# Kernel tuning notes

Measured on AMD Instinct MI355X. Metric: run time of the kernel, lower is better.

## Reference

```python
import jax, jax.numpy as jnp
import numpy as np

EPS = 1e-5
NUM_HEADS = 4


def _layer_norm(x, g, b):
    m = jnp.mean(x, axis=-1, keepdims=True)
    v = jnp.mean((x - m) ** 2, axis=-1, keepdims=True)
    return (x - m) / jnp.sqrt(v + EPS) * g + b


def setup_inputs() -> dict:
    key = jax.random.key(0)
    ks = jax.random.split(key, 32)
    B, N, ND, TD, L = 100000, 20, 128, 64, 2
    HD = 128  # num_heads * attention_dim
    CD = ND + TD  # 192
    s = 0.02
    inp = {
        "node_features": jax.random.normal(ks[0], (B, ND), jnp.float32),
        "neighbor_features": jax.random.normal(ks[1], (B, N, ND), jnp.float32),
        "node_times": jax.random.uniform(ks[2], (B,), jnp.float32),
        "neighbor_times": jax.random.uniform(ks[3], (B, N), jnp.float32),
        "time_freq": jax.random.normal(ks[4], (TD,), jnp.float32),
        "time_phase": jnp.zeros((TD,), jnp.float32),
        "Wq": jax.random.normal(ks[5], (L, CD, HD), jnp.float32) * s,
        "bq": jnp.zeros((L, HD), jnp.float32),
        "Wk": jax.random.normal(ks[6], (L, CD, HD), jnp.float32) * s,
        "bk": jnp.zeros((L, HD), jnp.float32),
        "Wv": jax.random.normal(ks[7], (L, CD, HD), jnp.float32) * s,
        "bv": jnp.zeros((L, HD), jnp.float32),
        "Wo": jax.random.normal(ks[8], (L, HD, ND), jnp.float32) * s,
        "bo": jnp.zeros((L, ND), jnp.float32),
        "W1": jax.random.normal(ks[9], (L, ND, 2 * ND), jnp.float32) * s,
        "b1": jnp.zeros((L, 2 * ND), jnp.float32),
        "W2": jax.random.normal(ks[10], (L, 2 * ND, ND), jnp.float32) * s,
        "b2": jnp.zeros((L, ND), jnp.float32),
        "g1": jnp.ones((L, ND), jnp.float32),
        "be1": jnp.zeros((L, ND), jnp.float32),
        "g2": jnp.ones((L, ND), jnp.float32),
        "be2": jnp.zeros((L, ND), jnp.float32),
        "Wc1": jax.random.normal(ks[11], (ND, ND // 2), jnp.float32) * s,
        "bc1": jnp.zeros((ND // 2,), jnp.float32),
        "Wc2": jax.random.normal(ks[12], (ND // 2, 1), jnp.float32) * s,
        "bc2": jnp.zeros((1,), jnp.float32),
        "mask": jax.random.randint(ks[13], (B, N), 0, 2, jnp.int32),
    }
    return inp


def reference(node_features, neighbor_features, node_times, neighbor_times,
              time_freq, time_phase, Wq, bq, Wk, bk, Wv, bv, Wo, bo,
              W1, b1, W2, b2, g1, be1, g2, be2, Wc1, bc1, Wc2, bc2, mask):
    L, _, HD = Wq.shape
    B, N, ND = neighbor_features.shape
    H = NUM_HEADS
    D = HD // H
    scale = 1.0 / np.sqrt(D).astype(np.float32)
    # time encodings (Bochner): cos(t * w + phi)
    tq = jnp.cos(node_times[:, None] * time_freq + time_phase)          # [B, TD]
    tk = jnp.cos(neighbor_times[..., None] * time_freq + time_phase)   # [B, N, TD]
    kcomb = jnp.concatenate([neighbor_features, tk], axis=-1)           # [B, N, CD]
    pad = (mask == 0)[:, None, :]                                       # [B, 1, N]
    x = node_features
    for l in range(L):
        qcomb = jnp.concatenate([x, tq], axis=-1)                       # [B, CD]
        q = (qcomb @ Wq[l] + bq[l]).reshape(B, H, D)
        k = (kcomb @ Wk[l] + bk[l]).reshape(B, N, H, D)
        v = (kcomb @ Wv[l] + bv[l]).reshape(B, N, H, D)
        scores = jnp.einsum('bhd,bnhd->bhn', q, k) * scale              # [B, H, N]
        scores = jnp.where(pad, jnp.float32(-1e9), scores)
        w = jax.nn.softmax(scores, axis=-1)
        a = jnp.einsum('bhn,bnhd->bhd', w, v).reshape(B, HD)
        attn = a @ Wo[l] + bo[l]                                        # [B, ND]
        x = _layer_norm(x + attn, g1[l], be1[l])
        ff = jax.nn.relu(x @ W1[l] + b1[l]) @ W2[l] + b2[l]
        x = _layer_norm(x + ff, g2[l], be2[l])
    h = jax.nn.relu(x @ Wc1 + bc1)
    return jax.nn.sigmoid(h @ Wc2 + bc2)                                # [B, 1]
```

## Files before the change

kernel.cpp:

```cpp
#include <hip/hip_runtime.h>

#define BB 100000
#define NN 20
#define ND 128
#define TD 64
#define CD 192
#define HD 128
#define NH 4
#define DH 32
#define NL 2

typedef __attribute__((ext_vector_type(8))) short bf16x8;
typedef __attribute__((ext_vector_type(4))) float f32x4;

static __device__ __forceinline__ float bf2f(unsigned short u) {
  return __uint_as_float(((unsigned)u) << 16);
}
static __device__ __forceinline__ unsigned short f2bf(float x) {
  unsigned b = __float_as_uint(x);
  return (unsigned short)((b + 0x7FFFu + ((b >> 16) & 1u)) >> 16);
}
static __device__ __forceinline__ bf16x8 load_a8(const float* p) {
  float4 a = *(const float4*)p, b = *(const float4*)(p + 4);
  bf16x8 r;
  r[0] = (short)f2bf(a.x); r[1] = (short)f2bf(a.y);
  r[2] = (short)f2bf(a.z); r[3] = (short)f2bf(a.w);
  r[4] = (short)f2bf(b.x); r[5] = (short)f2bf(b.y);
  r[6] = (short)f2bf(b.z); r[7] = (short)f2bf(b.w);
  return r;
}


__global__ __launch_bounds__(256) void conv_w(
    const float* __restrict__ Wq, const float* __restrict__ Wk,
    const float* __restrict__ Wv, const float* __restrict__ Wo,
    const float* __restrict__ W1, const float* __restrict__ W2,
    unsigned short* __restrict__ WF) {
  int t = blockIdx.x;
  int l = t / 304, tt = t % 304;
#pragma unroll
  for (int e = 0; e < 2; ++e) {
    int idx = threadIdx.x * 2 + e;
    int lane = idx >> 3, j = idx & 7;
    int wk = ((lane >> 4) << 3) + j;
    int c16 = lane & 15;
    float v;
    if (tt < 48) {
      int kt = tt >> 3, n2 = tt & 7;
      v = Wq[((size_t)l * CD + kt * 32 + wk) * HD + n2 * 16 + c16];
    } else if (tt < 96) {
      int t2 = tt - 48; int h = t2 / 12, n2 = t2 % 12;
      v = Wk[((size_t)l * CD + n2 * 16 + c16) * HD + h * 32 + wk];
    } else if (tt < 144) {
      int t2 = tt - 96; int h = t2 / 12, r2 = t2 % 12, kt = r2 >> 1, n2 = r2 & 1;
      v = Wv[((size_t)l * CD + kt * 32 + wk) * HD + h * 32 + n2 * 16 + c16];
    } else if (tt < 176) {
      int t2 = tt - 144; int kt = t2 >> 3, n2 = t2 & 7;
      v = Wo[((size_t)l * HD + kt * 32 + wk) * ND + n2 * 16 + c16];
    } else if (tt < 240) {
      int t2 = tt - 176; int kt = t2 >> 4, n2 = t2 & 15;
      v = W1[((size_t)l * ND + kt * 32 + wk) * (2 * ND) + n2 * 16 + c16];
    } else {
      int t2 = tt - 240; int kt = t2 >> 3, n2 = t2 & 7;
      v = W2[((size_t)l * 2 * ND + kt * 32 + wk) * ND + n2 * 16 + c16];
    }
    WF[(size_t)l * 155648 + (size_t)tt * 512 + idx] = f2bf(v);
  }
}

__global__ __launch_bounds__(256) void prep_tq(
    const float* __restrict__ ntime, const float* __restrict__ tf,
    const float* __restrict__ tp, float* __restrict__ tqf) {
  int i = blockIdx.x * 256 + threadIdx.x;
  int b = i >> 6, j = i & 63;
  tqf[i] = __cosf(ntime[b] * tf[j] + tp[j]);
}

__global__ __launch_bounds__(256) void prep_mb(const int* __restrict__ mask,
                                               unsigned* __restrict__ mb) {
  int e = blockIdx.x * 256 + threadIdx.x;
  if (e < BB) {
    unsigned m = 0;
    for (int n = 0; n < NN; ++n)
      m |= (mask[(size_t)e * NN + n] != 0 ? 1u : 0u) << n;
    mb[e] = m;
  }
}

template <int TN, int ABF, int OBF>
__global__ __launch_bounds__(256) void gemm16(
    const void* __restrict__ A, int lda,
    const float* __restrict__ A2, int lda2, int ksplit,
    const unsigned short* __restrict__ BF,
    int ktiles, int ntiles, int aKoffMul, int cColMul, int segBMul,
    const float* __restrict__ bias,
    void* __restrict__ C, int ldc, int relu) {
  const int tid = threadIdx.x;
  const int wv = tid >> 6, lane = tid & 63;
  const int NW = blockDim.x >> 6;
  const int m0 = blockIdx.x << 4;
  const int seg = blockIdx.y;
  const int arow = m0 + (lane & 15);
  const int kgrp = (lane >> 4) << 3;
  const int aK = seg * aKoffMul;
  const unsigned short* Bseg = BF + (size_t)seg * segBMul * 512;
  f32x4 acc[TN];
#pragma unroll
  for (int i = 0; i < TN; ++i) acc[i] = f32x4{0.f, 0.f, 0.f, 0.f};
  for (int kt = 0; kt < ktiles; ++kt) {
    bf16x8 af;
    if (kt * 32 >= ksplit) {
      af = load_a8(A2 + (size_t)arow * lda2 + (kt * 32 - ksplit) + kgrp);
    } else if (ABF) {
      af = *(const bf16x8*)((const unsigned short*)A + (size_t)arow * lda + aK +
                            kt * 32 + kgrp);
    } else {
      af = load_a8((const float*)A + (size_t)arow * lda + aK + kt * 32 + kgrp);
    }
#pragma unroll
    for (int i = 0; i < TN; ++i) {
      int nt = wv + NW * i;
      bf16x8 bf = *(const bf16x8*)(Bseg + (((size_t)(kt * ntiles + nt)) << 9) +
                                   (lane << 3));
      acc[i] = __builtin_amdgcn_mfma_f32_16x16x32_bf16(af, bf, acc[i], 0, 0, 0);
    }
  }
  const int crow = m0 + ((lane >> 4) << 2);
#pragma unroll
  for (int i = 0; i < TN; ++i) {
    int nt = wv + NW * i;
    int col = seg * cColMul + nt * 16 + (lane & 15);
    float bv = bias ? bias[col] : 0.f;
#pragma unroll
    for (int rr = 0; rr < 4; ++rr) {
      float v = acc[i][rr] + bv;
      if (relu) v = fmaxf(v, 0.f);
      if (OBF)
        ((unsigned short*)C)[(size_t)(crow + rr) * ldc + col] = f2bf(v);
      else
        ((float*)C)[(size_t)(crow + rr) * ldc + col] = v;
    }
  }
}

template <int ABF>
__global__ __launch_bounds__(256) void gemm_ln(
    const void* __restrict__ A, int lda, int ktiles,
    const unsigned short* __restrict__ BF,
    const float* __restrict__ bias, const float* __restrict__ res,
    const float* __restrict__ gamma, const float* __restrict__ beta,
    float* __restrict__ xout) {
  __shared__ float Cs[16][132];
  const int tid = threadIdx.x;
  const int wv = tid >> 6, lane = tid & 63;
  const int m0 = blockIdx.x << 4;
  const int arow = m0 + (lane & 15);
  const int kgrp = (lane >> 4) << 3;
  const int nt0 = wv, nt1 = wv + 4;
  f32x4 acc0 = {0.f, 0.f, 0.f, 0.f}, acc1 = {0.f, 0.f, 0.f, 0.f};
  for (int kt = 0; kt < ktiles; ++kt) {
    bf16x8 af;
    if (ABF)
      af = *(const bf16x8*)((const unsigned short*)A + (size_t)arow * lda +
                            kt * 32 + kgrp);
    else
      af = load_a8((const float*)A + (size_t)arow * lda + kt * 32 + kgrp);
    bf16x8 b0 = *(const bf16x8*)(BF + (((size_t)(kt * 8 + nt0)) << 9) + (lane << 3));
    bf16x8 b1 = *(const bf16x8*)(BF + (((size_t)(kt * 8 + nt1)) << 9) + (lane << 3));
    acc0 = __builtin_amdgcn_mfma_f32_16x16x32_bf16(af, b0, acc0, 0, 0, 0);
    acc1 = __builtin_amdgcn_mfma_f32_16x16x32_bf16(af, b1, acc1, 0, 0, 0);
  }
  {
    const int lrow = (lane >> 4) << 2;
    int c0 = nt0 * 16 + (lane & 15), c1 = nt1 * 16 + (lane & 15);
    float bv0 = bias[c0], bv1 = bias[c1];
#pragma unroll
    for (int rr = 0; rr < 4; ++rr) {
      Cs[lrow + rr][c0] = acc0[rr] + bv0;
      Cs[lrow + rr][c1] = acc1[rr] + bv1;
    }
  }
  __syncthreads();
#pragma unroll
  for (int rr = 0; rr < 4; ++rr) {
    int rw = wv * 4 + rr;
    size_t grow = (size_t)(m0 + rw) * ND;
    float y0 = Cs[rw][lane] + res[grow + lane];
    float y1 = Cs[rw][lane + 64] + res[grow + lane + 64];
    float s = y0 + y1, ss = y0 * y0 + y1 * y1;
#pragma unroll
    for (int off = 32; off > 0; off >>= 1) {
      s += __shfl_xor(s, off);
      ss += __shfl_xor(ss, off);
    }
    float mean = s * (1.f / ND);
    float var = ss * (1.f / ND) - mean * mean;
    float rstd = rsqrtf(var + 1e-5f);
    xout[grow + lane] = (y0 - mean) * rstd * gamma[lane] + beta[lane];
    xout[grow + lane + 64] =
        (y1 - mean) * rstd * gamma[lane + 64] + beta[lane + 64];
  }
}

template <int KCSRC>
__global__ __launch_bounds__(256) void attn_t(
    const float* __restrict__ nbf, const float* __restrict__ nbt,
    const float* __restrict__ tf, const float* __restrict__ tp,
    const unsigned short* __restrict__ kcf_in,
    unsigned short* __restrict__ kcf_out,
    const unsigned* __restrict__ mb, const unsigned short* __restrict__ r,
    unsigned short* __restrict__ u) {
  __shared__ __align__(16) unsigned short kcb[2][NN][200];
  __shared__ __align__(16) float rs[2][768];
  __shared__ __align__(16) float scs[2][NH][NN];
  __shared__ unsigned msks[2];
  const int tid = threadIdx.x;
  const size_t e0 = (size_t)blockIdx.x * 2;

  if (tid < 192) {
    uint4 v = *(const uint4*)(r + e0 * 768 + tid * 8);
    const unsigned short* pv = (const unsigned short*)&v;
    float* dst = &rs[0][0] + tid * 8;
#pragma unroll
    for (int k = 0; k < 8; ++k) dst[k] = bf2f(pv[k]);
  }
  if (KCSRC == 2) {
    for (int i = tid; i < 960; i += 256) {
      int el = i / 480, rem = i % 480;
      int n = rem / 24, q = rem % 24;
      *(uint4*)&kcb[el][n][q * 8] =
          *(const uint4*)&kcf_in[((e0 + el) * NN + n) * 192 + q * 8];
    }
  } else {
    for (int i = tid; i < 2 * NN * 32; i += 256) {
      int el = i / (NN * 32), rem = i % (NN * 32);
      int n = rem >> 5, cq = rem & 31;
      float4 v = *(const float4*)&nbf[((e0 + el) * NN + n) * ND + cq * 4];
      ushort4 o;
      o.x = f2bf(v.x); o.y = f2bf(v.y); o.z = f2bf(v.z); o.w = f2bf(v.w);
      *(ushort4*)&kcb[el][n][cq * 4] = o;
      if (KCSRC == 1)
        *(ushort4*)&kcf_out[((e0 + el) * NN + n) * 192 + cq * 4] = o;
    }
    for (int i = tid; i < 2 * NN * 32; i += 256) {
      int el = i / (NN * 32), rem = i % (NN * 32);
      int n = rem >> 5, jp = (rem & 31) * 2;
      float t = nbt[(e0 + el) * NN + n];
      unsigned a = f2bf(__cosf(t * tf[jp] + tp[jp]));
      unsigned b = f2bf(__cosf(t * tf[jp + 1] + tp[jp + 1]));
      unsigned w = a | (b << 16);
      *(unsigned*)&kcb[el][n][ND + jp] = w;
      if (KCSRC == 1)
        *(unsigned*)&kcf_out[((e0 + el) * NN + n) * 192 + ND + jp] = w;
    }
  }
  if (tid < 2) msks[tid] = mb[e0 + tid];
  __syncthreads();
  if (tid < 2 * NH * NN) {
    int el = tid / (NH * NN), rem = tid % (NH * NN);
    int h = rem / NN, n = rem % NN;
    const float* rp = &rs[el][h * CD];
    const unsigned short* kp = &kcb[el][n][0];
    float acc = 0.f;
    for (int c = 0; c < CD; c += 4) {
      float4 rv = *(const float4*)&rp[c];
      ushort4 kv = *(const ushort4*)&kp[c];
      acc += rv.x * bf2f(kv.x) + rv.y * bf2f(kv.y) + rv.z * bf2f(kv.z) +
             rv.w * bf2f(kv.w);
    }
    scs[el][h][n] =
        ((msks[el] >> n) & 1u) ? acc * 0.17677669529663687f : -1e9f;
  }
  __syncthreads();
  if (tid < 2 * NH) {
    int el = tid >> 2, h = tid & 3;
    float mx = -3.4e38f;
#pragma unroll
    for (int n = 0; n < NN; ++n) mx = fmaxf(mx, scs[el][h][n]);
    float ev[NN], s = 0.f;
#pragma unroll
    for (int n = 0; n < NN; ++n) { ev[n] = __expf(scs[el][h][n] - mx); s += ev[n]; }
    float inv = 1.f / s;
#pragma unroll
    for (int n = 0; n < NN; ++n) scs[el][h][n] = ev[n] * inv;
  }
  __syncthreads();
  for (int i = tid; i < 2 * NH * (CD / 4); i += 256) {
    int el = i / (NH * 48), rem = i % (NH * 48);
    int h = rem / 48, cq = (rem % 48) * 4;
    float a0 = 0.f, a1 = 0.f, a2 = 0.f, a3 = 0.f;
#pragma unroll
    for (int n = 0; n < NN; ++n) {
      float w = scs[el][h][n];
      ushort4 kv = *(const ushort4*)&kcb[el][n][cq];
      a0 += w * bf2f(kv.x); a1 += w * bf2f(kv.y);
      a2 += w * bf2f(kv.z); a3 += w * bf2f(kv.w);
    }
    ushort4 o;
    o.x = f2bf(a0); o.y = f2bf(a1); o.z = f2bf(a2); o.w = f2bf(a3);
    *(ushort4*)&u[(e0 + el) * 768 + h * 192 + cq] = o;
  }
}

__global__ __launch_bounds__(256) void cls_k(
    const float* __restrict__ xf, const float* __restrict__ Wc1,
    const float* __restrict__ bc1, const float* __restrict__ Wc2,
    const float* __restrict__ bc2, float* __restrict__ out) {
  __shared__ float xsh[4][128];
  const int tid = threadIdx.x;
  const size_t e0 = (size_t)blockIdx.x * 4;
  for (int i = tid; i < 512; i += 256) xsh[0][i] = xf[e0 * 128 + i];
  __syncthreads();
  int el = tid >> 6, lane = tid & 63;
  float acc = 0.f;
  for (int c = 0; c < 128; ++c) acc += xsh[el][c] * Wc1[c * 64 + lane];
  acc = fmaxf(acc + bc1[lane], 0.f);
  float p = acc * Wc2[lane];
#pragma unroll
  for (int off = 32; off > 0; off >>= 1) p += __shfl_xor(p, off);
  if (lane == 0) out[e0 + el] = 1.f / (1.f + expf(-(p + bc2[0])));
}

#define G 2
#define T 256
#define KCS 196
#define RUS 772

__global__ __launch_bounds__(T, 4) void tgat_fused(
    const float* __restrict__ nf, const float* __restrict__ nbf,
    const float* __restrict__ nt, const float* __restrict__ nbt,
    const float* __restrict__ tf, const float* __restrict__ tp,
    const float* __restrict__ Wq, const float* __restrict__ bq,
    const float* __restrict__ Wk,
    const float* __restrict__ Wv, const float* __restrict__ bv,
    const float* __restrict__ Wo, const float* __restrict__ bo,
    const float* __restrict__ W1, const float* __restrict__ b1,
    const float* __restrict__ W2, const float* __restrict__ b2,
    const float* __restrict__ g1, const float* __restrict__ be1,
    const float* __restrict__ g2, const float* __restrict__ be2,
    const float* __restrict__ Wc1, const float* __restrict__ bc1,
    const float* __restrict__ Wc2, const float* __restrict__ bc2,
    const int* __restrict__ mask,
    float* __restrict__ out) {
  __shared__ __align__(16) unsigned short kc[G][NN][KCS];
  __shared__ __align__(16) float xs[G][ND];
  __shared__ __align__(16) float tqs[G][TD];
  __shared__ __align__(16) float ys[G][HD];
  __shared__ __align__(16) float rus[G][RUS];
  __shared__ __align__(16) float scs[G][NH][NN];
  __shared__ __align__(16) float h1s[G][2 * ND];
  __shared__ __align__(16) unsigned msks[G];
  float* asv = &h1s[0][0];
  const int tid = threadIdx.x;
  const int b0 = blockIdx.x * G;
  {
    int g = tid >> 7, j = tid & 127;
    xs[g][j] = nf[(b0 + g) * ND + j];
  }
  if (tid < G * TD) {
    int g = tid >> 6, j = tid & 63;
    tqs[g][j] = __cosf(nt[b0 + g] * tf[j] + tp[j]);
  }
  if (tid < G) {
    unsigned m = 0;
    for (int n = 0; n < NN; ++n)
      m |= (mask[(b0 + tid) * NN + n] != 0 ? 1u : 0u) << n;
    msks[tid] = m;
  }
  for (int idx = tid; idx < G * NN * (ND / 4); idx += T) {
    int g = idx / (NN * 32), rem = idx % (NN * 32);
    int n = rem >> 5, cq = rem & 31;
    float4 v = *(const float4*)&nbf[(((b0 + g) * NN + n) * ND) + cq * 4];
    ushort4 o;
    o.x = f2bf(v.x); o.y = f2bf(v.y); o.z = f2bf(v.z); o.w = f2bf(v.w);
    *(ushort4*)&kc[g][n][cq * 4] = o;
  }
  for (int idx = tid; idx < G * NN * TD; idx += T) {
    int g = idx / (NN * TD), rem = idx % (NN * TD);
    int n = rem >> 6, j = rem & 63;
    kc[g][n][ND + j] = f2bf(__cosf(nbt[(b0 + g) * NN + n] * tf[j] + tp[j]));
  }
  __syncthreads();
  const float scale = 0.17677669529663687f;
  for (int l = 0; l < NL; ++l) {
    {
      int g = tid >> 7, j = tid & 127;
      const float* wq = Wq + (l * CD) * HD + j;
      float acc = bq[l * HD + j];
      for (int c = 0; c < CD; c += 4) {
        float4 qv = (c < ND) ? *(const float4*)&xs[g][c]
                             : *(const float4*)&tqs[g][c - ND];
        acc += qv.x * wq[(c + 0) * HD] + qv.y * wq[(c + 1) * HD] +
               qv.z * wq[(c + 2) * HD] + qv.w * wq[(c + 3) * HD];
      }
      ys[g][j] = acc;
    }
    __syncthreads();
    for (int rep = 0; rep < 3; ++rep) {
      int i = rep * T + tid;
      int h = i / CD;
      int c2 = i - h * CD;
      const float* wk = Wk + (l * CD + c2) * HD + h * DH;
      const float* yp0 = &ys[0][h * DH];
      const float* yp1 = &ys[1][h * DH];
      float a0 = 0.f, a1 = 0.f;
#pragma unroll
      for (int d = 0; d < DH; d += 4) {
        float4 w4 = *(const float4*)&wk[d];
        float4 y0 = *(const float4*)&yp0[d];
        float4 y1 = *(const float4*)&yp1[d];
        a0 += y0.x * w4.x + y0.y * w4.y + y0.z * w4.z + y0.w * w4.w;
        a1 += y1.x * w4.x + y1.y * w4.y + y1.z * w4.z + y1.w * w4.w;
      }
      rus[0][i] = a0;
      rus[1][i] = a1;
    }
    __syncthreads();
    if (tid < G * NH * NN) {
      int g = tid / (NH * NN), rem = tid % (NH * NN);
      int h = rem / NN, n = rem % NN;
      const float* rp = &rus[g][h * CD];
      const unsigned short* kp = &kc[g][n][0];
      float acc = 0.f;
      for (int c = 0; c < CD; c += 4) {
        float4 rv = *(const float4*)&rp[c];
        ushort4 kv = *(const ushort4*)&kp[c];
        acc += rv.x * bf2f(kv.x) + rv.y * bf2f(kv.y) + rv.z * bf2f(kv.z) +
               rv.w * bf2f(kv.w);
      }
      scs[g][h][n] = ((msks[g] >> n) & 1u) ? acc * scale : -1e9f;
    }
    __syncthreads();
    if (tid < G * NH) {
      int g = tid / NH, h = tid % NH;
      float mx = -3.4e38f;
#pragma unroll
      for (int n = 0; n < NN; ++n) mx = fmaxf(mx, scs[g][h][n]);
      float ev[NN], s = 0.f;
#pragma unroll
      for (int n = 0; n < NN; ++n) { ev[n] = __expf(scs[g][h][n] - mx); s += ev[n]; }
      float inv = 1.f / s;
#pragma unroll
      for (int n = 0; n < NN; ++n) scs[g][h][n] = ev[n] * inv;
    }
    __syncthreads();
    for (int flat = tid; flat < G * NH * (CD / 4); flat += T) {
      int g = flat / (NH * 48), iq = flat % (NH * 48);
      int h = iq / 48, c = (iq % 48) * 4;
      const unsigned short* kp = &kc[g][0][0];
      float a0 = 0.f, a1 = 0.f, a2 = 0.f, a3 = 0.f;
#pragma unroll
      for (int n = 0; n < NN; ++n) {
        float w = scs[g][h][n];
        ushort4 kv = *(const ushort4*)&kp[n * KCS + c];
        a0 += w * bf2f(kv.x); a1 += w * bf2f(kv.y);
        a2 += w * bf2f(kv.z); a3 += w * bf2f(kv.w);
      }
      *(float4*)&rus[g][h * CD + c] = make_float4(a0, a1, a2, a3);
    }
    __syncthreads();
    {
      int j = tid & (HD - 1);
      int g = tid >> 7;
      int h = j >> 5;
      const float* wv = Wv + (l * CD) * HD + j;
      float acc = 0.f;
      for (int c = 0; c < CD; c += 4) {
        float4 uv = *(const float4*)&rus[g][h * CD + c];
        acc += uv.x * wv[(c + 0) * HD] + uv.y * wv[(c + 1) * HD] +
               uv.z * wv[(c + 2) * HD] + uv.w * wv[(c + 3) * HD];
      }
      asv[g * HD + j] = acc + bv[l * HD + j];
    }
    __syncthreads();
    {
      int j = tid & (ND - 1);
      int g = tid >> 7;
      const float* wo = Wo + (l * HD) * ND + j;
      float acc = 0.f;
      for (int c = 0; c < HD; c += 4) {
        float4 av = *(const float4*)&asv[g * HD + c];
        acc += av.x * wo[(c + 0) * ND] + av.y * wo[(c + 1) * ND] +
               av.z * wo[(c + 2) * ND] + av.w * wo[(c + 3) * ND];
      }
      rus[g][j] = acc + bo[l * ND + j];
    }
    __syncthreads();
    if (tid < G * 64) {
      int g = tid >> 6, lane = tid & 63;
      float y0 = xs[g][lane] + rus[g][lane];
      float y1 = xs[g][lane + 64] + rus[g][lane + 64];
      float s = y0 + y1, ss = y0 * y0 + y1 * y1;
#pragma unroll
      for (int off = 32; off > 0; off >>= 1) {
        s += __shfl_xor(s, off);
        ss += __shfl_xor(ss, off);
      }
      float mean = s * (1.f / ND);
      float var = ss * (1.f / ND) - mean * mean;
      float rstd = rsqrtf(var + 1e-5f);
      xs[g][lane] = (y0 - mean) * rstd * g1[l * ND + lane] + be1[l * ND + lane];
      xs[g][lane + 64] =
          (y1 - mean) * rstd * g1[l * ND + lane + 64] + be1[l * ND + lane + 64];
    }
    __syncthreads();
    {
      int j = tid;
      const float* w1p = W1 + (l * ND) * (2 * ND) + j;
      float acc0 = 0.f, acc1 = 0.f;
      for (int c = 0; c < ND; c += 4) {
        float w0 = w1p[(c + 0) * 2 * ND], wa = w1p[(c + 1) * 2 * ND],
              w2 = w1p[(c + 2) * 2 * ND], w3 = w1p[(c + 3) * 2 * ND];
        float4 x0 = *(const float4*)&xs[0][c];
        float4 x1 = *(const float4*)&xs[1][c];
        acc0 += x0.x * w0 + x0.y * wa + x0.z * w2 + x0.w * w3;
        acc1 += x1.x * w0 + x1.y * wa + x1.z * w2 + x1.w * w3;
      }
      float b1v = b1[l * 2 * ND + j];
      h1s[0][j] = fmaxf(acc0 + b1v, 0.f);
      h1s[1][j] = fmaxf(acc1 + b1v, 0.f);
    }
    __syncthreads();
    {
      int j = tid & (ND - 1);
      int g = tid >> 7;
      const float* w2p = W2 + (l * 2 * ND) * ND + j;
      float acc = 0.f;
      for (int c = 0; c < 2 * ND; c += 4) {
        float4 hv = *(const float4*)&h1s[g][c];
        acc += hv.x * w2p[(c + 0) * ND] + hv.y * w2p[(c + 1) * ND] +
               hv.z * w2p[(c + 2) * ND] + hv.w * w2p[(c + 3) * ND];
      }
      rus[g][j] = acc + b2[l * ND + j];
    }
    __syncthreads();
    if (tid < G * 64) {
      int g = tid >> 6, lane = tid & 63;
      float y0 = xs[g][lane] + rus[g][lane];
      float y1 = xs[g][lane + 64] + rus[g][lane + 64];
      float s = y0 + y1, ss = y0 * y0 + y1 * y1;
#pragma unroll
      for (int off = 32; off > 0; off >>= 1) {
        s += __shfl_xor(s, off);
        ss += __shfl_xor(ss, off);
      }
      float mean = s * (1.f / ND);
      float var = ss * (1.f / ND) - mean * mean;
      float rstd = rsqrtf(var + 1e-5f);
      xs[g][lane] = (y0 - mean) * rstd * g2[l * ND + lane] + be2[l * ND + lane];
      xs[g][lane + 64] =
          (y1 - mean) * rstd * g2[l * ND + lane + 64] + be2[l * ND + lane + 64];
    }
    __syncthreads();
  }
  if (tid < G * 64) {
    int j = tid & 63;
    int g = tid >> 6;
    const float* wc = Wc1 + j;
    float acc = 0.f;
    for (int c = 0; c < ND; c += 4) {
      float4 xv = *(const float4*)&xs[g][c];
      acc += xv.x * wc[(c + 0) * 64] + xv.y * wc[(c + 1) * 64] +
             xv.z * wc[(c + 2) * 64] + xv.w * wc[(c + 3) * 64];
    }
    ((float*)scs)[g * 64 + j] = fmaxf(acc + bc1[j], 0.f);
  }
  __syncthreads();
  if (tid < G * 64) {
    int g = tid >> 6, lane = tid & 63;
    float p = ((float*)scs)[g * 64 + lane] * Wc2[lane];
#pragma unroll
    for (int off = 32; off > 0; off >>= 1) p += __shfl_xor(p, off);
    if (lane == 0) {
      float z = p + bc2[0];
      out[b0 + g] = 1.f / (1.f + expf(-z));
    }
  }
}

extern "C" void kernel_launch(void* const* d_in, const int* in_sizes, int n_in,
                              void* d_out, int out_size, void* d_ws,
                              size_t ws_size, hipStream_t stream) {
  (void)in_sizes; (void)n_in; (void)out_size;
  const float* nf  = (const float*)d_in[0];
  const float* nbf = (const float*)d_in[1];
  const float* ntm = (const float*)d_in[2];
  const float* nbt = (const float*)d_in[3];
  const float* tf  = (const float*)d_in[4];
  const float* tp  = (const float*)d_in[5];
  const float* Wq  = (const float*)d_in[6];
  const float* bq  = (const float*)d_in[7];
  const float* Wk  = (const float*)d_in[8];
  const float* Wv  = (const float*)d_in[10];
  const float* bv  = (const float*)d_in[11];
  const float* Wo  = (const float*)d_in[12];
  const float* bo  = (const float*)d_in[13];
  const float* W1  = (const float*)d_in[14];
  const float* b1  = (const float*)d_in[15];
  const float* W2  = (const float*)d_in[16];
  const float* b2  = (const float*)d_in[17];
  const float* g1  = (const float*)d_in[18];
  const float* be1 = (const float*)d_in[19];
  const float* g2  = (const float*)d_in[20];
  const float* be2 = (const float*)d_in[21];
  const float* Wc1 = (const float*)d_in[22];
  const float* bc1 = (const float*)d_in[23];
  const float* Wc2 = (const float*)d_in[24];
  const float* bc2 = (const float*)d_in[25];
  const int* mask  = (const int*)d_in[26];
  float* out = (float*)d_out;

  const size_t NEED_B = 333822592ull;
  const size_t NEED_A = 1101822592ull;
  if (ws_size >= NEED_B) {
    char* w = (char*)d_ws;
    unsigned short* WF = (unsigned short*)w;
    unsigned* mb = (unsigned*)(w + 622592);
    float* tqf = (float*)(w + 1022592);
    unsigned short* yb = (unsigned short*)(w + 26622592);
    unsigned short* rb = (unsigned short*)(w + 52222592);
    unsigned short* ab = (unsigned short*)(w + 205822592);
    unsigned short* h1b = (unsigned short*)(w + 231422592);
    float* xfb = (float*)(w + 282622592);
    unsigned short* kcf = (unsigned short*)(w + 333822592);
    const int tierA = (ws_size >= NEED_A);

    conv_w<<<608, 256, 0, stream>>>(Wq, Wk, Wv, Wo, W1, W2, WF);
    prep_tq<<<25000, 256, 0, stream>>>(ntm, tf, tp, tqf);
    prep_mb<<<(BB + 255) / 256, 256, 0, stream>>>(mask, mb);

    const float* xsrc = nf;
    for (int l = 0; l < NL; ++l) {
      const unsigned short* WFl = WF + (size_t)l * 155648;
      gemm16<2, 0, 1><<<dim3(6250, 1), 256, 0, stream>>>(
          xsrc, ND, tqf, TD, 128, WFl, 6, 8, 0, 0, 0, bq + l * HD, yb, HD, 0);
      gemm16<3, 1, 1><<<dim3(6250, 4), 256, 0, stream>>>(
          yb, HD, nullptr, 0, 1 << 30, WFl + 24576, 1, 12, DH, 192, 12,
          nullptr, rb, 768, 0);
      if (tierA) {
        if (l == 0)
          attn_t<1><<<50000, 256, 0, stream>>>(nbf, nbt, tf, tp, nullptr, kcf,
                                               mb, rb, rb);
        else
          attn_t<2><<<50000, 256, 0, stream>>>(nbf, nbt, tf, tp, kcf, nullptr,
                                               mb, rb, rb);
      } else {
        attn_t<0><<<50000, 256, 0, stream>>>(nbf, nbt, tf, tp, nullptr,
                                             nullptr, mb, rb, rb);
      }
      gemm16<1, 1, 1><<<dim3(6250, 4), 128, 0, stream>>>(
          rb, 768, nullptr, 0, 1 << 30, WFl + 49152, 6, 2, 192, DH, 12,
          bv + l * HD, ab, HD, 0);
      gemm_ln<1><<<6250, 256, 0, stream>>>(ab, HD, 4, WFl + 73728, bo + l * ND,
                                           xsrc, g1 + l * ND, be1 + l * ND,
                                           xfb);
      gemm16<4, 0, 1><<<dim3(6250, 1), 256, 0, stream>>>(
          xfb, ND, nullptr, 0, 1 << 30, WFl + 90112, 4, 16, 0, 0, 0,
          b1 + l * 2 * ND, h1b, 2 * ND, 1);
      gemm_ln<1><<<6250, 256, 0, stream>>>(h1b, 2 * ND, 8, WFl + 122880,
                                           b2 + l * ND, xfb, g2 + l * ND,
                                           be2 + l * ND, xfb);
      xsrc = xfb;
    }
    cls_k<<<25000, 256, 0, stream>>>(xfb, Wc1, bc1, Wc2, bc2, out);
  } else {
    tgat_fused<<<BB / G, T, 0, stream>>>(nf, nbf, ntm, nbt, tf, tp, Wq, bq, Wk,
                                         Wv, bv, Wo, bo, W1, b1, W2, b2, g1,
                                         be1, g2, be2, Wc1, bc1, Wc2, bc2,
                                         mask, out);
  }
}
```

Baseline: 1.408 ms.

## Fold Wq·Wk and Wv·Wo into precomputed weights and fuse classifier into final LN

```diff
diff --git a/kernel.cpp b/kernel.cpp
--- a/kernel.cpp
+++ b/kernel.cpp
@@ -9,6 +9,7 @@
 #define NH 4
 #define DH 32
 #define NL 2
+#define WLS 311296
 
 typedef __attribute__((ext_vector_type(8))) short bf16x8;
 typedef __attribute__((ext_vector_type(4))) float f32x4;
@@ -29,15 +30,79 @@
   r[6] = (short)f2bf(b.z); r[7] = (short)f2bf(b.w);
   return r;
 }
-
-
-__global__ __launch_bounds__(256) void conv_w(
+static __device__ __forceinline__ int fragidx(int wk, int c16) {
+  return (((wk >> 3) << 4) | c16) * 8 + (wk & 7);
+}
+
+
+__global__ __launch_bounds__(192) void precomp_M(
     const float* __restrict__ Wq, const float* __restrict__ Wk,
+    unsigned short* __restrict__ WF) {
+  int e = blockIdx.x;
+  int c1 = e % CD;
+  int h = (e / CD) % NH;
+  int l = e / (CD * NH);
+  int c2 = threadIdx.x;
+  const float* wq = Wq + ((size_t)l * CD + c1) * HD + h * DH;
+  const float* wk = Wk + ((size_t)l * CD + c2) * HD + h * DH;
+  float acc = 0.f;
+#pragma unroll
+  for (int d = 0; d < DH; ++d) acc += wq[d] * wk[d];
+  int n = h * CD + c2;
+  int nt = n >> 4, c16 = n & 15;
+  int kt = c1 >> 5, wk2 = c1 & 31;
+  WF[(size_t)l * WLS + (size_t)(kt * 48 + nt) * 512 + fragidx(wk2, c16)] =
+      f2bf(acc);
+}
+
+__global__ __launch_bounds__(192) void precomp_pk(
+    const float* __restrict__ bq, const float* __restrict__ Wk,
+    float* __restrict__ pk) {
+  int e = blockIdx.x;
+  int h = e % NH, l = e / NH;
+  int c2 = threadIdx.x;
+  const float* bqp = bq + (size_t)l * HD + h * DH;
+  const float* wk = Wk + ((size_t)l * CD + c2) * HD + h * DH;
+  float acc = 0.f;
+#pragma unroll
+  for (int d = 0; d < DH; ++d) acc += bqp[d] * wk[d];
+  pk[(size_t)l * 768 + h * CD + c2] = acc;
+}
+
+__global__ __launch_bounds__(128) void precomp_WC(
     const float* __restrict__ Wv, const float* __restrict__ Wo,
+    unsigned short* __restrict__ WF) {
+  int e = blockIdx.x;
+  int k = e % 768, l = e / 768;
+  int c = k % CD, h = k / CD;
+  int j = threadIdx.x;
+  const float* wv = Wv + ((size_t)l * CD + c) * HD + h * DH;
+  const float* wo = Wo + ((size_t)l * HD + h * DH) * ND + j;
+  float acc = 0.f;
+#pragma unroll
+  for (int d = 0; d < DH; ++d) acc += wv[d] * wo[(size_t)d * ND];
+  int kt = k >> 5, wk2 = k & 31;
+  int nt = j >> 4, c16 = j & 15;
+  WF[(size_t)l * WLS + 147456 + (size_t)(kt * 8 + nt) * 512 +
+     fragidx(wk2, c16)] = f2bf(acc);
+}
+
+__global__ __launch_bounds__(128) void precomp_bC(
+    const float* __restrict__ bv, const float* __restrict__ bo,
+    const float* __restrict__ Wo, float* __restrict__ bC) {
+  int l = blockIdx.x;
+  int j = threadIdx.x;
+  float acc = bo[(size_t)l * ND + j];
+  for (int k = 0; k < HD; ++k)
+    acc += bv[(size_t)l * HD + k] * Wo[((size_t)l * HD + k) * ND + j];
+  bC[(size_t)l * ND + j] = acc;
+}
+
+__global__ __launch_bounds__(256) void conv_w2(
     const float* __restrict__ W1, const float* __restrict__ W2,
     unsigned short* __restrict__ WF) {
   int t = blockIdx.x;
-  int l = t / 304, tt = t % 304;
+  int l = t >> 7, tt = t & 127;
 #pragma unroll
   for (int e = 0; e < 2; ++e) {
     int idx = threadIdx.x * 2 + e;
@@ -45,26 +110,18 @@
     int wk = ((lane >> 4) << 3) + j;
     int c16 = lane & 15;
     float v;
-    if (tt < 48) {
-      int kt = tt >> 3, n2 = tt & 7;
-      v = Wq[((size_t)l * CD + kt * 32 + wk) * HD + n2 * 16 + c16];
-    } else if (tt < 96) {
-      int t2 = tt - 48; int h = t2 / 12, n2 = t2 % 12;
-      v = Wk[((size_t)l * CD + n2 * 16 + c16) * HD + h * 32 + wk];
-    } else if (tt < 144) {
-      int t2 = tt - 96; int h = t2 / 12, r2 = t2 % 12, kt = r2 >> 1, n2 = r2 & 1;
-      v = Wv[((size_t)l * CD + kt * 32 + wk) * HD + h * 32 + n2 * 16 + c16];
-    } else if (tt < 176) {
-      int t2 = tt - 144; int kt = t2 >> 3, n2 = t2 & 7;
-      v = Wo[((size_t)l * HD + kt * 32 + wk) * ND + n2 * 16 + c16];
-    } else if (tt < 240) {
-      int t2 = tt - 176; int kt = t2 >> 4, n2 = t2 & 15;
+    size_t dst;
+    if (tt < 64) {
+      int kt = tt >> 4, n2 = tt & 15;
       v = W1[((size_t)l * ND + kt * 32 + wk) * (2 * ND) + n2 * 16 + c16];
+      dst = (size_t)l * WLS + 245760 + (size_t)tt * 512 + idx;
     } else {
-      int t2 = tt - 240; int kt = t2 >> 3, n2 = t2 & 7;
+      int t2 = tt - 64;
+      int kt = t2 >> 3, n2 = t2 & 7;
       v = W2[((size_t)l * 2 * ND + kt * 32 + wk) * ND + n2 * 16 + c16];
-    }
-    WF[(size_t)l * 155648 + (size_t)tt * 512 + idx] = f2bf(v);
+      dst = (size_t)l * WLS + 278528 + (size_t)t2 * 512 + idx;
+    }
+    WF[dst] = f2bf(v);
   }
 }
 
@@ -92,18 +149,15 @@
     const void* __restrict__ A, int lda,
     const float* __restrict__ A2, int lda2, int ksplit,
     const unsigned short* __restrict__ BF,
-    int ktiles, int ntiles, int aKoffMul, int cColMul, int segBMul,
+    int ktiles, int ntiles,
     const float* __restrict__ bias,
     void* __restrict__ C, int ldc, int relu) {
   const int tid = threadIdx.x;
   const int wv = tid >> 6, lane = tid & 63;
   const int NW = blockDim.x >> 6;
   const int m0 = blockIdx.x << 4;
-  const int seg = blockIdx.y;
   const int arow = m0 + (lane & 15);
   const int kgrp = (lane >> 4) << 3;
-  const int aK = seg * aKoffMul;
-  const unsigned short* Bseg = BF + (size_t)seg * segBMul * 512;
   f32x4 acc[TN];
 #pragma unroll
   for (int i = 0; i < TN; ++i) acc[i] = f32x4{0.f, 0.f, 0.f, 0.f};
@@ -112,15 +166,15 @@
     if (kt * 32 >= ksplit) {
       af = load_a8(A2 + (size_t)arow * lda2 + (kt * 32 - ksplit) + kgrp);
     } else if (ABF) {
-      af = *(const bf16x8*)((const unsigned short*)A + (size_t)arow * lda + aK +
+      af = *(const bf16x8*)((const unsigned short*)A + (size_t)arow * lda +
                             kt * 32 + kgrp);
     } else {
-      af = load_a8((const float*)A + (size_t)arow * lda + aK + kt * 32 + kgrp);
+      af = load_a8((const float*)A + (size_t)arow * lda + kt * 32 + kgrp);
     }
 #pragma unroll
     for (int i = 0; i < TN; ++i) {
       int nt = wv + NW * i;
-      bf16x8 bf = *(const bf16x8*)(Bseg + (((size_t)(kt * ntiles + nt)) << 9) +
+      bf16x8 bf = *(const bf16x8*)(BF + (((size_t)(kt * ntiles + nt)) << 9) +
                                    (lane << 3));
       acc[i] = __builtin_amdgcn_mfma_f32_16x16x32_bf16(af, bf, acc[i], 0, 0, 0);
     }
@@ -129,7 +183,7 @@
 #pragma unroll
   for (int i = 0; i < TN; ++i) {
     int nt = wv + NW * i;
-    int col = seg * cColMul + nt * 16 + (lane & 15);
+    int col = nt * 16 + (lane & 15);
     float bv = bias ? bias[col] : 0.f;
 #pragma unroll
     for (int rr = 0; rr < 4; ++rr) {
@@ -143,14 +197,18 @@
   }
 }
 
-template <int ABF>
+template <int ABF, int CLS>
 __global__ __launch_bounds__(256) void gemm_ln(
     const void* __restrict__ A, int lda, int ktiles,
     const unsigned short* __restrict__ BF,
     const float* __restrict__ bias, const float* __restrict__ res,
     const float* __restrict__ gamma, const float* __restrict__ beta,
-    float* __restrict__ xout) {
+    float* __restrict__ xout,
+    const float* __restrict__ Wc1, const float* __restrict__ bc1,
+    const float* __restrict__ Wc2, const float* __restrict__ bc2,
+    float* __restrict__ out) {
   __shared__ float Cs[16][132];
+  __shared__ float hsh[16][64];
   const int tid = threadIdx.x;
   const int wv = tid >> 6, lane = tid & 63;
   const int m0 = blockIdx.x << 4;
@@ -196,18 +254,42 @@
     float mean = s * (1.f / ND);
     float var = ss * (1.f / ND) - mean * mean;
     float rstd = rsqrtf(var + 1e-5f);
-    xout[grow + lane] = (y0 - mean) * rstd * gamma[lane] + beta[lane];
-    xout[grow + lane + 64] =
-        (y1 - mean) * rstd * gamma[lane + 64] + beta[lane + 64];
-  }
-}
-
-template <int KCSRC>
-__global__ __launch_bounds__(256) void attn_t(
+    float x0 = (y0 - mean) * rstd * gamma[lane] + beta[lane];
+    float x1 = (y1 - mean) * rstd * gamma[lane + 64] + beta[lane + 64];
+    if (CLS) {
+      Cs[rw][lane] = x0;
+      Cs[rw][lane + 64] = x1;
+    } else {
+      xout[grow + lane] = x0;
+      xout[grow + lane + 64] = x1;
+    }
+  }
+  if (CLS) {
+    __syncthreads();
+#pragma unroll
+    for (int rep = 0; rep < 4; ++rep) {
+      int idx = rep * 256 + tid;
+      int row = idx >> 6, j = idx & 63;
+      float acc = 0.f;
+      for (int c = 0; c < ND; ++c) acc += Cs[row][c] * Wc1[c * 64 + j];
+      hsh[row][j] = fmaxf(acc + bc1[j], 0.f);
+    }
+    __syncthreads();
+#pragma unroll
+    for (int rr = 0; rr < 4; ++rr) {
+      int row = wv * 4 + rr;
+      float p = hsh[row][lane] * Wc2[lane];
+#pragma unroll
+      for (int off = 32; off > 0; off >>= 1) p += __shfl_xor(p, off);
+      if (lane == 0)
+        out[m0 + row] = 1.f / (1.f + expf(-(p + bc2[0])));
+    }
+  }
+}
+
+__global__ __launch_bounds__(256) void attn_b(
     const float* __restrict__ nbf, const float* __restrict__ nbt,
     const float* __restrict__ tf, const float* __restrict__ tp,
-    const unsigned short* __restrict__ kcf_in,
-    unsigned short* __restrict__ kcf_out,
     const unsigned* __restrict__ mb, const unsigned short* __restrict__ r,
     unsigned short* __restrict__ u) {
   __shared__ __align__(16) unsigned short kcb[2][NN][200];
@@ -224,35 +306,21 @@
 #pragma unroll
     for (int k = 0; k < 8; ++k) dst[k] = bf2f(pv[k]);
   }
-  if (KCSRC == 2) {
-    for (int i = tid; i < 960; i += 256) {
-      int el = i / 480, rem = i % 480;
-      int n = rem / 24, q = rem % 24;
-      *(uint4*)&kcb[el][n][q * 8] =
-          *(const uint4*)&kcf_in[((e0 + el) * NN + n) * 192 + q * 8];
-    }
-  } else {
-    for (int i = tid; i < 2 * NN * 32; i += 256) {
-      int el = i / (NN * 32), rem = i % (NN * 32);
-      int n = rem >> 5, cq = rem & 31;
-      float4 v = *(const float4*)&nbf[((e0 + el) * NN + n) * ND + cq * 4];
-      ushort4 o;
-      o.x = f2bf(v.x); o.y = f2bf(v.y); o.z = f2bf(v.z); o.w = f2bf(v.w);
-      *(ushort4*)&kcb[el][n][cq * 4] = o;
-      if (KCSRC == 1)
-        *(ushort4*)&kcf_out[((e0 + el) * NN + n) * 192 + cq * 4] = o;
-    }
-    for (int i = tid; i < 2 * NN * 32; i += 256) {
-      int el = i / (NN * 32), rem = i % (NN * 32);
-      int n = rem >> 5, jp = (rem & 31) * 2;
-      float t = nbt[(e0 + el) * NN + n];
-      unsigned a = f2bf(__cosf(t * tf[jp] + tp[jp]));
-      unsigned b = f2bf(__cosf(t * tf[jp + 1] + tp[jp + 1]));
-      unsigned w = a | (b << 16);
-      *(unsigned*)&kcb[el][n][ND + jp] = w;
-      if (KCSRC == 1)
-        *(unsigned*)&kcf_out[((e0 + el) * NN + n) * 192 + ND + jp] = w;
-    }
+  for (int i = tid; i < 2 * NN * 32; i += 256) {
+    int el = i / (NN * 32), rem = i % (NN * 32);
+    int n = rem >> 5, cq = rem & 31;
+    float4 v = *(const float4*)&nbf[((e0 + el) * NN + n) * ND + cq * 4];
+    ushort4 o;
+    o.x = f2bf(v.x); o.y = f2bf(v.y); o.z = f2bf(v.z); o.w = f2bf(v.w);
+    *(ushort4*)&kcb[el][n][cq * 4] = o;
+  }
+  for (int i = tid; i < 2 * NN * 32; i += 256) {
+    int el = i / (NN * 32), rem = i % (NN * 32);
+    int n = rem >> 5, jp = (rem & 31) * 2;
+    float t = nbt[(e0 + el) * NN + n];
+    unsigned a = f2bf(__cosf(t * tf[jp] + tp[jp]));
+    unsigned b = f2bf(__cosf(t * tf[jp + 1] + tp[jp + 1]));
+    *(unsigned*)&kcb[el][n][ND + jp] = a | (b << 16);
   }
   if (tid < 2) msks[tid] = mb[e0 + tid];
   __syncthreads();
@@ -298,27 +366,8 @@
     }
     ushort4 o;
     o.x = f2bf(a0); o.y = f2bf(a1); o.z = f2bf(a2); o.w = f2bf(a3);
-    *(ushort4*)&u[(e0 + el) * 768 + h * 192 + cq] = o;
-  }
-}
-
-__global__ __launch_bounds__(256) void cls_k(
-    const float* __restrict__ xf, const float* __restrict__ Wc1,
-    const float* __restrict__ bc1, const float* __restrict__ Wc2,
-    const float* __restrict__ bc2, float* __restrict__ out) {
-  __shared__ float xsh[4][128];
-  const int tid = threadIdx.x;
-  const size_t e0 = (size_t)blockIdx.x * 4;
-  for (int i = tid; i < 512; i += 256) xsh[0][i] = xf[e0 * 128 + i];
-  __syncthreads();
-  int el = tid >> 6, lane = tid & 63;
-  float acc = 0.f;
-  for (int c = 0; c < 128; ++c) acc += xsh[el][c] * Wc1[c * 64 + lane];
-  acc = fmaxf(acc + bc1[lane], 0.f);
-  float p = acc * Wc2[lane];
-#pragma unroll
-  for (int off = 32; off > 0; off >>= 1) p += __shfl_xor(p, off);
-  if (lane == 0) out[e0 + el] = 1.f / (1.f + expf(-(p + bc2[0])));
+    *(ushort4*)&u[(e0 + el) * 768 + h * CD + cq] = o;
+  }
 }
 
 #define G 2
@@ -610,59 +659,48 @@
   const int* mask  = (const int*)d_in[26];
   float* out = (float*)d_out;
 
-  const size_t NEED_B = 333822592ull;
-  const size_t NEED_A = 1101822592ull;
-  if (ws_size >= NEED_B) {
+  const size_t NEED = 283252352ull;
+  if (ws_size >= NEED) {
     char* w = (char*)d_ws;
     unsigned short* WF = (unsigned short*)w;
-    unsigned* mb = (unsigned*)(w + 622592);
-    float* tqf = (float*)(w + 1022592);
-    unsigned short* yb = (unsigned short*)(w + 26622592);
-    unsigned short* rb = (unsigned short*)(w + 52222592);
-    unsigned short* ab = (unsigned short*)(w + 205822592);
-    unsigned short* h1b = (unsigned short*)(w + 231422592);
-    float* xfb = (float*)(w + 282622592);
-    unsigned short* kcf = (unsigned short*)(w + 333822592);
-    const int tierA = (ws_size >= NEED_A);
-
-    conv_w<<<608, 256, 0, stream>>>(Wq, Wk, Wv, Wo, W1, W2, WF);
+    float* pk = (float*)(w + 1245184);
+    float* bC = (float*)(w + 1251328);
+    unsigned* mb = (unsigned*)(w + 1252352);
+    float* tqf = (float*)(w + 1652352);
+    unsigned short* rb = (unsigned short*)(w + 27252352);
+    unsigned short* h1b = (unsigned short*)(w + 180852352);
+    float* xfb = (float*)(w + 232052352);
+
+    precomp_M<<<NL * NH * CD, CD, 0, stream>>>(Wq, Wk, WF);
+    precomp_pk<<<NL * NH, CD, 0, stream>>>(bq, Wk, pk);
+    precomp_WC<<<NL * 768, ND, 0, stream>>>(Wv, Wo, WF);
+    precomp_bC<<<NL, ND, 0, stream>>>(bv, bo, Wo, bC);
+    conv_w2<<<256, 256, 0, stream>>>(W1, W2, WF);
     prep_tq<<<25000, 256, 0, stream>>>(ntm, tf, tp, tqf);
     prep_mb<<<(BB + 255) / 256, 256, 0, stream>>>(mask, mb);
 
     const float* xsrc = nf;
     for (int l = 0; l < NL; ++l) {
-      const unsigned short* WFl = WF + (size_t)l * 155648;
-      gemm16<2, 0, 1><<<dim3(6250, 1), 256, 0, stream>>>(
-          xsrc, ND, tqf, TD, 128, WFl, 6, 8, 0, 0, 0, bq + l * HD, yb, HD, 0);
-      gemm16<3, 1, 1><<<dim3(6250, 4), 256, 0, stream>>>(
-          yb, HD, nullptr, 0, 1 << 30, WFl + 24576, 1, 12, DH, 192, 12,
-          nullptr, rb, 768, 0);
-      if (tierA) {
-        if (l == 0)
-          attn_t<1><<<50000, 256, 0, stream>>>(nbf, nbt, tf, tp, nullptr, kcf,
-                                               mb, rb, rb);
-        else
-          attn_t<2><<<50000, 256, 0, stream>>>(nbf, nbt, tf, tp, kcf, nullptr,
-                                               mb, rb, rb);
-      } else {
-        attn_t<0><<<50000, 256, 0, stream>>>(nbf, nbt, tf, tp, nullptr,
-                                             nullptr, mb, rb, rb);
-      }
-      gemm16<1, 1, 1><<<dim3(6250, 4), 128, 0, stream>>>(
-          rb, 768, nullptr, 0, 1 << 30, WFl + 49152, 6, 2, 192, DH, 12,
-          bv + l * HD, ab, HD, 0);
-      gemm_ln<1><<<6250, 256, 0, stream>>>(ab, HD, 4, WFl + 73728, bo + l * ND,
-                                           xsrc, g1 + l * ND, be1 + l * ND,
-                                           xfb);
-      gemm16<4, 0, 1><<<dim3(6250, 1), 256, 0, stream>>>(
-          xfb, ND, nullptr, 0, 1 << 30, WFl + 90112, 4, 16, 0, 0, 0,
+      const unsigned short* WFl = WF + (size_t)l * WLS;
+      gemm16<12, 0, 1><<<6250, 256, 0, stream>>>(
+          xsrc, ND, tqf, TD, 128, WFl, 6, 48, pk + l * 768, rb, 768, 0);
+      attn_b<<<50000, 256, 0, stream>>>(nbf, nbt, tf, tp, mb, rb, rb);
+      gemm_ln<1, 0><<<6250, 256, 0, stream>>>(
+          rb, 768, 24, WFl + 147456, bC + l * ND, xsrc, g1 + l * ND,
+          be1 + l * ND, xfb, nullptr, nullptr, nullptr, nullptr, nullptr);
+      gemm16<4, 0, 1><<<6250, 256, 0, stream>>>(
+          xfb, ND, nullptr, 0, 1 << 30, WFl + 245760, 4, 16,
           b1 + l * 2 * ND, h1b, 2 * ND, 1);
-      gemm_ln<1><<<6250, 256, 0, stream>>>(h1b, 2 * ND, 8, WFl + 122880,
-                                           b2 + l * ND, xfb, g2 + l * ND,
-                                           be2 + l * ND, xfb);
+      if (l == NL - 1)
+        gemm_ln<1, 1><<<6250, 256, 0, stream>>>(
+            h1b, 2 * ND, 8, WFl + 278528, b2 + l * ND, xfb, g2 + l * ND,
+            be2 + l * ND, xfb, Wc1, bc1, Wc2, bc2, out);
+      else
+        gemm_ln<1, 0><<<6250, 256, 0, stream>>>(
+            h1b, 2 * ND, 8, WFl + 278528, b2 + l * ND, xfb, g2 + l * ND,
+            be2 + l * ND, xfb, nullptr, nullptr, nullptr, nullptr, nullptr);
       xsrc = xfb;
     }
-    cls_k<<<25000, 256, 0, stream>>>(xfb, Wc1, bc1, Wc2, bc2, out);
   } else {
     tgat_fused<<<BB / G, T, 0, stream>>>(nf, nbf, ntm, nbt, tf, tp, Wq, bq, Wk,
                                          Wv, bv, Wo, bo, W1, b1, W2, b2, g1,
```

New measurement: 1.565 ms. +11.1%, slower.

## Fuse classifier head into final LayerNorm GEMM and drop cached bf16 key buffer

Applied to the files above, without the earlier changes.

```diff
diff --git a/kernel.cpp b/kernel.cpp
--- a/kernel.cpp
+++ b/kernel.cpp
@@ -143,14 +143,18 @@
   }
 }
 
-template <int ABF>
+template <int ABF, int CLS>
 __global__ __launch_bounds__(256) void gemm_ln(
     const void* __restrict__ A, int lda, int ktiles,
     const unsigned short* __restrict__ BF,
     const float* __restrict__ bias, const float* __restrict__ res,
     const float* __restrict__ gamma, const float* __restrict__ beta,
-    float* __restrict__ xout) {
+    float* __restrict__ xout,
+    const float* __restrict__ Wc1, const float* __restrict__ bc1,
+    const float* __restrict__ Wc2, const float* __restrict__ bc2,
+    float* __restrict__ out) {
   __shared__ float Cs[16][132];
+  __shared__ float hsh[CLS ? 16 : 1][64];
   const int tid = threadIdx.x;
   const int wv = tid >> 6, lane = tid & 63;
   const int m0 = blockIdx.x << 4;
@@ -196,18 +200,42 @@
     float mean = s * (1.f / ND);
     float var = ss * (1.f / ND) - mean * mean;
     float rstd = rsqrtf(var + 1e-5f);
-    xout[grow + lane] = (y0 - mean) * rstd * gamma[lane] + beta[lane];
-    xout[grow + lane + 64] =
-        (y1 - mean) * rstd * gamma[lane + 64] + beta[lane + 64];
-  }
-}
-
-template <int KCSRC>
-__global__ __launch_bounds__(256) void attn_t(
+    float x0 = (y0 - mean) * rstd * gamma[lane] + beta[lane];
+    float x1 = (y1 - mean) * rstd * gamma[lane + 64] + beta[lane + 64];
+    if (CLS) {
+      Cs[rw][lane] = x0;
+      Cs[rw][lane + 64] = x1;
+    } else {
+      xout[grow + lane] = x0;
+      xout[grow + lane + 64] = x1;
+    }
+  }
+  if (CLS) {
+    __syncthreads();
+#pragma unroll
+    for (int rep = 0; rep < 4; ++rep) {
+      int idx = rep * 256 + tid;
+      int row = idx >> 6, j = idx & 63;
+      float a = 0.f;
+      for (int c = 0; c < ND; ++c) a += Cs[row][c] * Wc1[c * 64 + j];
+      hsh[row][j] = fmaxf(a + bc1[j], 0.f);
+    }
+    __syncthreads();
+#pragma unroll
+    for (int rr = 0; rr < 4; ++rr) {
+      int row = wv * 4 + rr;
+      float p = hsh[row][lane] * Wc2[lane];
+#pragma unroll
+      for (int off = 32; off > 0; off >>= 1) p += __shfl_xor(p, off);
+      if (lane == 0)
+        out[m0 + row] = 1.f / (1.f + expf(-(p + bc2[0])));
+    }
+  }
+}
+
+__global__ __launch_bounds__(256) void attn_b(
     const float* __restrict__ nbf, const float* __restrict__ nbt,
     const float* __restrict__ tf, const float* __restrict__ tp,
-    const unsigned short* __restrict__ kcf_in,
-    unsigned short* __restrict__ kcf_out,
     const unsigned* __restrict__ mb, const unsigned short* __restrict__ r,
     unsigned short* __restrict__ u) {
   __shared__ __align__(16) unsigned short kcb[2][NN][200];
@@ -224,35 +252,21 @@
 #pragma unroll
     for (int k = 0; k < 8; ++k) dst[k] = bf2f(pv[k]);
   }
-  if (KCSRC == 2) {
-    for (int i = tid; i < 960; i += 256) {
-      int el = i / 480, rem = i % 480;
-      int n = rem / 24, q = rem % 24;
-      *(uint4*)&kcb[el][n][q * 8] =
-          *(const uint4*)&kcf_in[((e0 + el) * NN + n) * 192 + q * 8];
-    }
-  } else {
-    for (int i = tid; i < 2 * NN * 32; i += 256) {
-      int el = i / (NN * 32), rem = i % (NN * 32);
-      int n = rem >> 5, cq = rem & 31;
-      float4 v = *(const float4*)&nbf[((e0 + el) * NN + n) * ND + cq * 4];
-      ushort4 o;
-      o.x = f2bf(v.x); o.y = f2bf(v.y); o.z = f2bf(v.z); o.w = f2bf(v.w);
-      *(ushort4*)&kcb[el][n][cq * 4] = o;
-      if (KCSRC == 1)
-        *(ushort4*)&kcf_out[((e0 + el) * NN + n) * 192 + cq * 4] = o;
-    }
-    for (int i = tid; i < 2 * NN * 32; i += 256) {
-      int el = i / (NN * 32), rem = i % (NN * 32);
-      int n = rem >> 5, jp = (rem & 31) * 2;
-      float t = nbt[(e0 + el) * NN + n];
-      unsigned a = f2bf(__cosf(t * tf[jp] + tp[jp]));
-      unsigned b = f2bf(__cosf(t * tf[jp + 1] + tp[jp + 1]));
-      unsigned w = a | (b << 16);
-      *(unsigned*)&kcb[el][n][ND + jp] = w;
-      if (KCSRC == 1)
-        *(unsigned*)&kcf_out[((e0 + el) * NN + n) * 192 + ND + jp] = w;
-    }
+  for (int i = tid; i < 2 * NN * 32; i += 256) {
+    int el = i / (NN * 32), rem = i % (NN * 32);
+    int n = rem >> 5, cq = rem & 31;
+    float4 v = *(const float4*)&nbf[((e0 + el) * NN + n) * ND + cq * 4];
+    ushort4 o;
+    o.x = f2bf(v.x); o.y = f2bf(v.y); o.z = f2bf(v.z); o.w = f2bf(v.w);
+    *(ushort4*)&kcb[el][n][cq * 4] = o;
+  }
+  for (int i = tid; i < 2 * NN * 32; i += 256) {
+    int el = i / (NN * 32), rem = i % (NN * 32);
+    int n = rem >> 5, jp = (rem & 31) * 2;
+    float t = nbt[(e0 + el) * NN + n];
+    unsigned a = f2bf(__cosf(t * tf[jp] + tp[jp]));
+    unsigned b = f2bf(__cosf(t * tf[jp + 1] + tp[jp + 1]));
+    *(unsigned*)&kcb[el][n][ND + jp] = a | (b << 16);
   }
   if (tid < 2) msks[tid] = mb[e0 + tid];
   __syncthreads();
@@ -298,27 +312,8 @@
     }
     ushort4 o;
     o.x = f2bf(a0); o.y = f2bf(a1); o.z = f2bf(a2); o.w = f2bf(a3);
-    *(ushort4*)&u[(e0 + el) * 768 + h * 192 + cq] = o;
-  }
-}
-
-__global__ __launch_bounds__(256) void cls_k(
-    const float* __restrict__ xf, const float* __restrict__ Wc1,
-    const float* __restrict__ bc1, const float* __restrict__ Wc2,
-    const float* __restrict__ bc2, float* __restrict__ out) {
-  __shared__ float xsh[4][128];
-  const int tid = threadIdx.x;
-  const size_t e0 = (size_t)blockIdx.x * 4;
-  for (int i = tid; i < 512; i += 256) xsh[0][i] = xf[e0 * 128 + i];
-  __syncthreads();
-  int el = tid >> 6, lane = tid & 63;
-  float acc = 0.f;
-  for (int c = 0; c < 128; ++c) acc += xsh[el][c] * Wc1[c * 64 + lane];
-  acc = fmaxf(acc + bc1[lane], 0.f);
-  float p = acc * Wc2[lane];
-#pragma unroll
-  for (int off = 32; off > 0; off >>= 1) p += __shfl_xor(p, off);
-  if (lane == 0) out[e0 + el] = 1.f / (1.f + expf(-(p + bc2[0])));
+    *(ushort4*)&u[(e0 + el) * 768 + h * CD + cq] = o;
+  }
 }
 
 #define G 2
@@ -610,9 +605,8 @@
   const int* mask  = (const int*)d_in[26];
   float* out = (float*)d_out;
 
-  const size_t NEED_B = 333822592ull;
-  const size_t NEED_A = 1101822592ull;
-  if (ws_size >= NEED_B) {
+  const size_t NEED = 333822592ull;
+  if (ws_size >= NEED) {
     char* w = (char*)d_ws;
     unsigned short* WF = (unsigned short*)w;
     unsigned* mb = (unsigned*)(w + 622592);
@@ -622,8 +616,6 @@
     unsigned short* ab = (unsigned short*)(w + 205822592);
     unsigned short* h1b = (unsigned short*)(w + 231422592);
     float* xfb = (float*)(w + 282622592);
-    unsigned short* kcf = (unsigned short*)(w + 333822592);
-    const int tierA = (ws_size >= NEED_A);
 
     conv_w<<<608, 256, 0, stream>>>(Wq, Wk, Wv, Wo, W1, W2, WF);
     prep_tq<<<25000, 256, 0, stream>>>(ntm, tf, tp, tqf);
@@ -637,32 +629,26 @@
       gemm16<3, 1, 1><<<dim3(6250, 4), 256, 0, stream>>>(
           yb, HD, nullptr, 0, 1 << 30, WFl + 24576, 1, 12, DH, 192, 12,
           nullptr, rb, 768, 0);
-      if (tierA) {
-        if (l == 0)
-          attn_t<1><<<50000, 256, 0, stream>>>(nbf, nbt, tf, tp, nullptr, kcf,
-                                               mb, rb, rb);
-        else
-          attn_t<2><<<50000, 256, 0, stream>>>(nbf, nbt, tf, tp, kcf, nullptr,
-                                               mb, rb, rb);
-      } else {
-        attn_t<0><<<50000, 256, 0, stream>>>(nbf, nbt, tf, tp, nullptr,
-                                             nullptr, mb, rb, rb);
-      }
+      attn_b<<<50000, 256, 0, stream>>>(nbf, nbt, tf, tp, mb, rb, rb);
       gemm16<1, 1, 1><<<dim3(6250, 4), 128, 0, stream>>>(
           rb, 768, nullptr, 0, 1 << 30, WFl + 49152, 6, 2, 192, DH, 12,
           bv + l * HD, ab, HD, 0);
-      gemm_ln<1><<<6250, 256, 0, stream>>>(ab, HD, 4, WFl + 73728, bo + l * ND,
-                                           xsrc, g1 + l * ND, be1 + l * ND,
-                                           xfb);
+      gemm_ln<1, 0><<<6250, 256, 0, stream>>>(
+          ab, HD, 4, WFl + 73728, bo + l * ND, xsrc, g1 + l * ND,
+          be1 + l * ND, xfb, nullptr, nullptr, nullptr, nullptr, nullptr);
       gemm16<4, 0, 1><<<dim3(6250, 1), 256, 0, stream>>>(
           xfb, ND, nullptr, 0, 1 << 30, WFl + 90112, 4, 16, 0, 0, 0,
           b1 + l * 2 * ND, h1b, 2 * ND, 1);
-      gemm_ln<1><<<6250, 256, 0, stream>>>(h1b, 2 * ND, 8, WFl + 122880,
-                                           b2 + l * ND, xfb, g2 + l * ND,
-                                           be2 + l * ND, xfb);
+      if (l == NL - 1)
+        gemm_ln<1, 1><<<6250, 256, 0, stream>>>(
+            h1b, 2 * ND, 8, WFl + 122880, b2 + l * ND, xfb, g2 + l * ND,
+            be2 + l * ND, xfb, Wc1, bc1, Wc2, bc2, out);
+      else
+        gemm_ln<1, 0><<<6250, 256, 0, stream>>>(
+            h1b, 2 * ND, 8, WFl + 122880, b2 + l * ND, xfb, g2 + l * ND,
+            be2 + l * ND, xfb, nullptr, nullptr, nullptr, nullptr, nullptr);
       xsrc = xfb;
     }
-    cls_k<<<25000, 256, 0, stream>>>(xfb, Wc1, bc1, Wc2, bc2, out);
   } else {
     tgat_fused<<<BB / G, T, 0, stream>>>(nf, nbf, ntm, nbt, tf, tp, Wq, bq, Wk,
                                          Wv, bv, Wo, bo, W1, b1, W2, b2, g1,
```

Result: no change. 1.405 ms (-0.3%).
